# Kernel optimization log

Measured on AMD Instinct MI355X. Metric: run time of the kernel, lower is better.

Reference implementation:

```python
import jax, jax.numpy as jnp
import numpy as np
from math import factorial

MAXL = 5
TAUS = [8, 8, 8, 8, 8, 8]
OUT_TAUS = [8, 8, 8, 8, 8, 8]
BM_EPS = 1e-5
BATCH = 1024


def _cg_coeff(l1, l2, l, m1, m2, m):
    # Standard Clebsch-Gordan coefficient <l1 m1 l2 m2 | l m> (Racah formula).
    if m1 + m2 != m:
        return 0.0
    f = factorial
    pre = ((2 * l + 1) * f(l + l1 - l2) * f(l - l1 + l2) * f(l1 + l2 - l) / f(l1 + l2 + l + 1)) ** 0.5
    pre *= (f(l + m) * f(l - m) * f(l1 - m1) * f(l1 + m1) * f(l2 - m2) * f(l2 + m2)) ** 0.5
    s = 0.0
    for k in range(0, l1 + l2 - l + 1):
        ds = [k, l1 + l2 - l - k, l1 - m1 - k, l2 + m2 - k, l - l2 + m1 + k, l - l1 - m2 + k]
        if min(ds) < 0:
            continue
        d = 1.0
        for v in ds:
            d *= f(v)
        s += (-1.0) ** k / d
    return pre * s


def _cg_block(l1, l2, l):
    C = np.zeros((2 * l + 1, 2 * l1 + 1, 2 * l2 + 1), dtype=np.float32)
    for m in range(-l, l + 1):
        for m1 in range(-l1, l1 + 1):
            m2 = m - m1
            if -l2 <= m2 <= l2:
                C[m + l, m1 + l1, m2 + l2] = _cg_coeff(l1, l2, l, m1, m2, m)
    return C


# Triple enumeration order matches cal_middle_taus (l1 outer, l2, then l).
TRIPLES = []
for _l1 in range(MAXL + 1):
    for _l2 in range(_l1 + 1):
        for _l in range(_l1 - _l2, min(_l1 + _l2, MAXL) + 1):
            TRIPLES.append((_l1, _l2, _l))
CG_BLOCKS = [jnp.asarray(_cg_block(*t)) for t in TRIPLES]

MIDDLE_TAUS = np.zeros(MAXL + 1, dtype=np.int64)
for (_l1, _l2, _l) in TRIPLES:
    MIDDLE_TAUS[_l] += TAUS[_l1] * TAUS[_l2]
IN_LEN = int(sum(TAUS[l] * (2 * l + 1) for l in range(MAXL + 1)))    # 288
OUT_LEN = int(sum(OUT_TAUS[l] * (2 * l + 1) for l in range(MAXL + 1)))  # 288
WLEN = int(sum(OUT_TAUS[l] * int(MIDDLE_TAUS[l]) for l in range(MAXL + 1)))  # 35328
STD_LEN = int(MIDDLE_TAUS.sum())  # 4416


def _forward(activations, weights, moving_std):
    B = activations.shape[0]
    act = activations[..., 0] + 1j * activations[..., 1]  # [B, IN_LEN] complex64
    # split into per-degree blocks F[l]: [B, tau_l, 2l+1]
    F = []
    st = 0
    for l in range(MAXL + 1):
        n = TAUS[l] * (2 * l + 1)
        F.append(act[:, st:st + n].reshape(B, TAUS[l], 2 * l + 1))
        st += n
    # CG tensor product: one fragment per (l1,l2,l) triple, grouped by output degree l
    mids = [[] for _ in range(MAXL + 1)]
    for (l1, l2, l), C in zip(TRIPLES, CG_BLOCKS):
        frag = jnp.einsum('mac,bta,bsc->btsm', C.astype(act.dtype), F[l1], F[l2])
        mids[l].append(frag.reshape(B, TAUS[l1] * TAUS[l2], 2 * l + 1))
    # per-fragment batchnorm (divide by running std) + per-degree complex mixing
    outs = []
    so = 0
    wo = 0
    for l in range(MAXL + 1):
        mid = jnp.concatenate(mids[l], axis=1)  # [B, middle_taus[l], 2l+1]
        nt = int(MIDDLE_TAUS[l])
        std = moving_std[so:so + nt]
        so += nt
        mid = mid / (std + BM_EPS)[None, :, None]
        nw = OUT_TAUS[l] * nt
        wl = weights[wo:wo + nw]
        wo += nw
        Wc = (wl[:, 0] + 1j * wl[:, 1]).reshape(OUT_TAUS[l], nt)
        out = jnp.einsum('ot,btm->bom', Wc, mid)  # [B, out_taus[l], 2l+1]
        outs.append(out.reshape(B, OUT_TAUS[l] * (2 * l + 1)))
    oc = jnp.concatenate(outs, axis=1)  # [B, OUT_LEN] complex
    return jnp.stack([oc.real, oc.imag], axis=-1)  # [B, OUT_LEN, 2]


def setup_inputs() -> dict:
    key = jax.random.key(0)
    k1, k2, k3 = jax.random.split(key, 3)
    activations = jax.random.normal(k1, (BATCH, IN_LEN, 2), dtype=jnp.float32)
    weights = 0.05 * jax.random.uniform(k2, (WLEN, 2), dtype=jnp.float32)
    moving_std = 0.1 + 0.9 * jax.random.uniform(k3, (STD_LEN,), dtype=jnp.float32)
    return {"activations": activations, "weights": weights, "moving_std": moving_std}


def reference(activations, weights, moving_std):
    return _forward(activations, weights, moving_std)
```

## Files before the change

### kernel.cpp

```cpp
#include <hip/hip_runtime.h>
#include <hip/hip_bf16.h>
#include <utility>


constexpr int NTRIP = 69;
constexpr int NL    = 6;
constexpr int BATCH = 1024;
constexpr int ROW   = 288;
constexpr int MID_LDS = 4224;

struct Meta {
    int tl1[NTRIP], tl2[NTRIP], tll[NTRIP];
    int tf1[NTRIP], tf2[NTRIP];
    int ttloc[NTRIP];
    int trip_of_l[NL][16];
    int ntrips[NL];
    int mid_tau[NL], std_off[NL], w_off[NL], f_l[NL];
    int nch[NL];
    int ch_start[NL][2], ch_cnt[NL][2];
    int wave_of[NL][16];
};

constexpr Meta build_meta() {
    Meta m{};
    int fl[NL] = {};
    {
        int acc = 0;
        for (int l = 0; l < NL; l++) { fl[l] = acc; m.f_l[l] = acc; acc += 8 * (2 * l + 1); }
    }
    int idx = 0;
    for (int l1 = 0; l1 <= 5; l1++)
        for (int l2 = 0; l2 <= l1; l2++) {
            int lmax = (l1 + l2 < 5) ? (l1 + l2) : 5;
            for (int l = l1 - l2; l <= lmax; l++) {
                m.tl1[idx] = l1; m.tl2[idx] = l2; m.tll[idx] = l;
                m.tf1[idx] = fl[l1]; m.tf2[idx] = fl[l2];
                m.ttloc[idx] = 64 * m.ntrips[l];
                m.trip_of_l[l][m.ntrips[l]] = idx;
                m.ntrips[l]++;
                idx++;
            }
        }
    int so = 0, wo = 0;
    for (int l = 0; l < NL; l++) {
        m.mid_tau[l] = 64 * m.ntrips[l];
        m.std_off[l] = so; so += m.mid_tau[l];
        m.w_off[l]   = wo; wo += 8 * m.mid_tau[l];
    }
    for (int l = 0; l < NL; l++) {
        const int TW = 2 * l + 1;
        const int maxslot = MID_LDS / (64 * TW);
        const int ntl = m.ntrips[l];
        const int nch = (ntl + maxslot - 1) / maxslot;
        m.nch[l] = nch;
        int done = 0;
        for (int c = 0; c < nch; c++) {
            int cnt = (ntl - done + (nch - c) - 1) / (nch - c);
            m.ch_start[l][c] = done; m.ch_cnt[l][c] = cnt; done += cnt;
        }
        for (int c = 0; c < nch; c++) {
            const int s0 = m.ch_start[l][c], cnt = m.ch_cnt[l][c];
            int cost[16] = {}; bool asg[16] = {};
            for (int i = 0; i < cnt; i++) {
                int trip = m.trip_of_l[l][s0 + i];
                int l1 = m.tl1[trip], l2 = m.tl2[trip];
                int tc = 0;
                for (int mi = 0; mi < TW; mi++) {
                    int base = mi - l;
                    int lo = base + l1 - l2; if (lo < 0) lo = 0;
                    int hi = base + l1 + l2; if (hi > 2 * l1) hi = 2 * l1;
                    tc += hi - lo + 1;
                }
                cost[i] = tc * 6 + (2 * l1 + 1 + 2 * l2 + 1) * 2;
            }
            int load[4] = {};
            for (int k = 0; k < cnt; k++) {
                int best = -1, bc = -1;
                for (int i = 0; i < cnt; i++)
                    if (!asg[i] && cost[i] > bc) { bc = cost[i]; best = i; }
                asg[best] = true;
                int wsel = 0;
                for (int w2 = 1; w2 < 4; w2++) if (load[w2] < load[wsel]) wsel = w2;
                m.wave_of[l][s0 + best] = wsel;
                load[wsel] += bc;
            }
        }
    }
    return m;
}

constexpr Meta MT = build_meta();
constexpr int WLEN = 35328;
static_assert(MT.w_off[5] + 8 * MT.mid_tau[5] == WLEN, "wlen");
static_assert(MT.std_off[5] + MT.mid_tau[5] == 4416, "stdlen");

constexpr double cfact(int n) {
    double r = 1.0;
    for (int i = 2; i <= n; i++) r *= (double)i;
    return r;
}
constexpr double csqrt(double x) {
    double g = x > 1.0 ? x : 1.0;
    for (int i = 0; i < 100; i++) g = 0.5 * (g + x / g);
    return g;
}
constexpr float cg_coeff(int l1, int l2, int l, int m1, int m2, int m) {
    if (m1 + m2 != m) return 0.0f;
    double pre = csqrt((double)(2 * l + 1) * cfact(l + l1 - l2) * cfact(l - l1 + l2) *
                       cfact(l1 + l2 - l) / cfact(l1 + l2 + l + 1));
    pre *= csqrt(cfact(l + m) * cfact(l - m) * cfact(l1 - m1) * cfact(l1 + m1) *
                 cfact(l2 - m2) * cfact(l2 + m2));
    double s = 0.0;
    for (int k = 0; k <= l1 + l2 - l; k++) {
        int d0 = k, d1 = l1 + l2 - l - k, d2 = l1 - m1 - k;
        int d3 = l2 + m2 - k, d4 = l - l2 + m1 + k, d5 = l - l1 - m2 + k;
        if (d0 < 0 || d1 < 0 || d2 < 0 || d3 < 0 || d4 < 0 || d5 < 0) continue;
        double den = cfact(d0) * cfact(d1) * cfact(d2) * cfact(d3) * cfact(d4) * cfact(d5);
        s += ((k & 1) ? -1.0 : 1.0) / den;
    }
    return (float)(pre * s);
}

template <int... Is, class F>
__device__ __forceinline__ void static_for_impl(std::integer_sequence<int, Is...>, F&& f) {
    (f(std::integral_constant<int, Is>{}), ...);
}
template <int N, class F>
__device__ __forceinline__ void static_for(F&& f) {
    static_for_impl(std::make_integer_sequence<int, N>{}, (F&&)f);
}

template <int L>
__device__ __forceinline__ void process_l(int b, int tid,
                                          const float2* __restrict__ F,
                                          float2* __restrict__ mid,
                                          const float2* __restrict__ w,
                                          const float* __restrict__ stdv,
                                          float2* __restrict__ out) {
    constexpr int TW  = 2 * L + 1;
    constexpr int NCH = MT.nch[L];
    constexpr int NT  = MT.mid_tau[L];

    const int wid  = tid >> 6;
    const int lane = tid & 63;
    const int t = lane >> 3, s = lane & 7;

    float2 acc0[TW], acc1[TW];
#pragma unroll
    for (int i = 0; i < TW; i++) { acc0[i] = make_float2(0.f, 0.f); acc1[i] = make_float2(0.f, 0.f); }

    static_for<NCH>([&](auto CHc) {
        constexpr int CH  = decltype(CHc)::value;
        constexpr int S0  = MT.ch_start[L][CH];
        constexpr int CNT = MT.ch_cnt[L][CH];
        constexpr int CT  = CNT * 64;
        static_assert(CT * TW <= MID_LDS, "chunk fits");

        __syncthreads();

        static_for<CNT>([&](auto SIc) {
            constexpr int SI   = S0 + decltype(SIc)::value;
            constexpr int TRIP = MT.trip_of_l[L][SI];
            constexpr int L1   = MT.tl1[TRIP];
            constexpr int L2v  = MT.tl2[TRIP];
            constexpr int N1   = 2 * L1 + 1, N2 = 2 * L2v + 1;
            if (MT.wave_of[L][SI] == wid) {
                const float inv = 1.0f /
                    (stdv[MT.std_off[L] + MT.ttloc[TRIP] + lane] + 1e-5f);
                const float2* F1 = F + MT.tf1[TRIP] + t * N1;
                const float2* F2 = F + MT.tf2[TRIP] + s * N2;
                float2 f1[N1], f2[N2];
#pragma unroll
                for (int i = 0; i < N1; i++) f1[i] = F1[i];
#pragma unroll
                for (int i = 0; i < N2; i++) f2[i] = F2[i];
                const int Tloc = (MT.ttloc[TRIP] - S0 * 64) + lane;
                static_for<TW>([&](auto MIc) {
                    constexpr int MI   = decltype(MIc)::value;
                    constexpr int BASE = MI - L;
                    constexpr int LO_  = BASE + L1 - L2v;
                    constexpr int LO   = LO_ < 0 ? 0 : LO_;
                    constexpr int HI_  = BASE + L1 + L2v;
                    constexpr int HI   = HI_ > 2 * L1 ? 2 * L1 : HI_;
                    float re = 0.f, im = 0.f;
                    static_for<HI - LO + 1>([&](auto Kc) {
                        constexpr int AI = LO + decltype(Kc)::value;
                        constexpr int CI = BASE + L1 + L2v - AI;
                        constexpr float cv = cg_coeff(L1, L2v, L, AI - L1, CI - L2v, BASE);
                        if constexpr (cv != 0.0f) {
                            const float2 a = f1[AI], c2 = f2[CI];
                            re = fmaf(cv, fmaf(-a.y, c2.y, a.x * c2.x), re);
                            im = fmaf(cv, fmaf(a.y, c2.x, a.x * c2.y), im);
                        }
                    });
                    mid[MI * CT + Tloc] = make_float2(re * inv, im * inv);
                });
            }
        });
        __syncthreads();

        {
            constexpr int NIT = (CT + 127) / 128;
            const float2* W0 = w + MT.w_off[L] + wid * NT + S0 * 64;
            const float2* W1 = w + MT.w_off[L] + (wid + 4) * NT + S0 * 64;
            float4 wA[NIT], wB[NIT];
            static_for<NIT>([&](auto Ic) {
                constexpr int I = decltype(Ic)::value;
                const int T = lane * 2 + I * 128;
                if constexpr ((I + 1) * 128 <= CT) {
                    wA[I] = *reinterpret_cast<const float4*>(W0 + T);
                    wB[I] = *reinterpret_cast<const float4*>(W1 + T);
                } else {
                    if (T < CT) {
                        wA[I] = *reinterpret_cast<const float4*>(W0 + T);
                        wB[I] = *reinterpret_cast<const float4*>(W1 + T);
                    }
                }
            });
            static_for<NIT>([&](auto Ic) {
                constexpr int I = decltype(Ic)::value;
                const int T = lane * 2 + I * 128;
                const float4 w0 = wA[I], w1 = wB[I];
                auto body = [&]() {
#pragma unroll
                    for (int mi = 0; mi < TW; mi++) {
                        const float4 mv = *reinterpret_cast<const float4*>(mid + mi * CT + T);
                        acc0[mi].x = fmaf(w0.x, mv.x, fmaf(-w0.y, mv.y,
                                      fmaf(w0.z, mv.z, fmaf(-w0.w, mv.w, acc0[mi].x))));
                        acc0[mi].y = fmaf(w0.x, mv.y, fmaf(w0.y, mv.x,
                                      fmaf(w0.z, mv.w, fmaf(w0.w, mv.z, acc0[mi].y))));
                        acc1[mi].x = fmaf(w1.x, mv.x, fmaf(-w1.y, mv.y,
                                      fmaf(w1.z, mv.z, fmaf(-w1.w, mv.w, acc1[mi].x))));
                        acc1[mi].y = fmaf(w1.x, mv.y, fmaf(w1.y, mv.x,
                                      fmaf(w1.z, mv.w, fmaf(w1.w, mv.z, acc1[mi].y))));
                    }
                };
                if constexpr ((I + 1) * 128 <= CT) body();
                else { if (T < CT) body(); }
            });
        }
    });

    const bool lo = (lane < 32);
    float2 red[TW];
#pragma unroll
    for (int mi = 0; mi < TW; mi++) {
        float gx = lo ? acc1[mi].x : acc0[mi].x;
        float gy = lo ? acc1[mi].y : acc0[mi].y;
        float rx = (lo ? acc0[mi].x : acc1[mi].x) + __shfl_xor(gx, 32, 64);
        float ry = (lo ? acc0[mi].y : acc1[mi].y) + __shfl_xor(gy, 32, 64);
#pragma unroll
        for (int off = 16; off >= 1; off >>= 1) {
            rx += __shfl_xor(rx, off, 64);
            ry += __shfl_xor(ry, off, 64);
        }
        red[mi] = make_float2(rx, ry);
    }
    if (lane == 0 || lane == 32) {
        const int o = wid + (lo ? 0 : 4);
        float2* orow = out + (size_t)b * ROW + MT.f_l[L] + o * TW;
#pragma unroll
        for (int mi = 0; mi < TW; mi++) orow[mi] = red[mi];
    }
}

__global__ __launch_bounds__(256, 4) void fup_main(const float2* __restrict__ act,
                                                   const float2* __restrict__ w,
                                                   const float* __restrict__ stdv,
                                                   float2* __restrict__ out) {
    __shared__ float2 F[ROW];
    __shared__ __align__(16) float2 mid[MID_LDS];
    const int b = blockIdx.x;
    const int tid = threadIdx.x;
    const float2* arow = act + (size_t)b * ROW;
    for (int i = tid; i < ROW; i += 256) F[i] = arow[i];
    process_l<0>(b, tid, F, mid, w, stdv, out);
    process_l<1>(b, tid, F, mid, w, stdv, out);
    process_l<2>(b, tid, F, mid, w, stdv, out);
    process_l<3>(b, tid, F, mid, w, stdv, out);
    process_l<4>(b, tid, F, mid, w, stdv, out);
    process_l<5>(b, tid, F, mid, w, stdv, out);
}

extern "C" void kernel_launch(void* const* d_in, const int* in_sizes, int n_in,
                              void* d_out, int out_size, void* d_ws, size_t ws_size,
                              hipStream_t stream) {
    const float2* act  = (const float2*)d_in[0];
    const float2* wts  = (const float2*)d_in[1];
    const float*  stdv = (const float*)d_in[2];
    float2* out = (float2*)d_out;
    (void)d_ws; (void)ws_size;

    hipLaunchKernelGGL(fup_main, dim3(BATCH), dim3(256), 0, stream,
                       act, wts, stdv, out);
}
```

Measured before the change: 138.2 us.

## Split each batch row across two blocks by degree group, halve mid LDS

Each batch row is now processed by two blocks: one handles output degrees 0,1,2,5 and the other handles 3,4, with the groups balanced by chunk count. The grid doubles, the mid LDS buffer is halved, and launch bounds rise to 8 blocks per CU to increase occupancy and parallelism. The weight-load loop becomes a runtime loop instead of a fully prefetched static_for, which reduces register pressure but drops the early weight-load batching. Each block redundantly loads the activation row, and the chunking metadata is widened to support smaller chunks.

After: 343.1 us. +148.3%, slower.

```diff
diff --git a/kernel.cpp b/kernel.cpp
--- a/kernel.cpp
+++ b/kernel.cpp
@@ -7,7 +7,7 @@
 constexpr int NL    = 6;
 constexpr int BATCH = 1024;
 constexpr int ROW   = 288;
-constexpr int MID_LDS = 4224;
+constexpr int MID_LDS = 2112;
 
 struct Meta {
     int tl1[NTRIP], tl2[NTRIP], tll[NTRIP];
@@ -17,7 +17,7 @@
     int ntrips[NL];
     int mid_tau[NL], std_off[NL], w_off[NL], f_l[NL];
     int nch[NL];
-    int ch_start[NL][2], ch_cnt[NL][2];
+    int ch_start[NL][8], ch_cnt[NL][8];
     int wave_of[NL][16];
 };
 
@@ -93,6 +93,8 @@
 constexpr int WLEN = 35328;
 static_assert(MT.w_off[5] + 8 * MT.mid_tau[5] == WLEN, "wlen");
 static_assert(MT.std_off[5] + MT.mid_tau[5] == 4416, "stdlen");
+static_assert(MT.nch[0] + MT.nch[1] + MT.nch[2] + MT.nch[5] == 9, "grpA");
+static_assert(MT.nch[3] + MT.nch[4] == 9, "grpB");
 
 constexpr double cfact(int n) {
     double r = 1.0;
@@ -200,44 +202,24 @@
         __syncthreads();
 
         {
-            constexpr int NIT = (CT + 127) / 128;
             const float2* W0 = w + MT.w_off[L] + wid * NT + S0 * 64;
             const float2* W1 = w + MT.w_off[L] + (wid + 4) * NT + S0 * 64;
-            float4 wA[NIT], wB[NIT];
-            static_for<NIT>([&](auto Ic) {
-                constexpr int I = decltype(Ic)::value;
-                const int T = lane * 2 + I * 128;
-                if constexpr ((I + 1) * 128 <= CT) {
-                    wA[I] = *reinterpret_cast<const float4*>(W0 + T);
-                    wB[I] = *reinterpret_cast<const float4*>(W1 + T);
-                } else {
-                    if (T < CT) {
-                        wA[I] = *reinterpret_cast<const float4*>(W0 + T);
-                        wB[I] = *reinterpret_cast<const float4*>(W1 + T);
-                    }
+            for (int T = lane * 2; T < CT; T += 128) {
+                const float4 w0 = *reinterpret_cast<const float4*>(W0 + T);
+                const float4 w1 = *reinterpret_cast<const float4*>(W1 + T);
+#pragma unroll
+                for (int mi = 0; mi < TW; mi++) {
+                    const float4 mv = *reinterpret_cast<const float4*>(mid + mi * CT + T);
+                    acc0[mi].x = fmaf(w0.x, mv.x, fmaf(-w0.y, mv.y,
+                                  fmaf(w0.z, mv.z, fmaf(-w0.w, mv.w, acc0[mi].x))));
+                    acc0[mi].y = fmaf(w0.x, mv.y, fmaf(w0.y, mv.x,
+                                  fmaf(w0.z, mv.w, fmaf(w0.w, mv.z, acc0[mi].y))));
+                    acc1[mi].x = fmaf(w1.x, mv.x, fmaf(-w1.y, mv.y,
+                                  fmaf(w1.z, mv.z, fmaf(-w1.w, mv.w, acc1[mi].x))));
+                    acc1[mi].y = fmaf(w1.x, mv.y, fmaf(w1.y, mv.x,
+                                  fmaf(w1.z, mv.w, fmaf(w1.w, mv.z, acc1[mi].y))));
                 }
-            });
-            static_for<NIT>([&](auto Ic) {
-                constexpr int I = decltype(Ic)::value;
-                const int T = lane * 2 + I * 128;
-                const float4 w0 = wA[I], w1 = wB[I];
-                auto body = [&]() {
-#pragma unroll
-                    for (int mi = 0; mi < TW; mi++) {
-                        const float4 mv = *reinterpret_cast<const float4*>(mid + mi * CT + T);
-                        acc0[mi].x = fmaf(w0.x, mv.x, fmaf(-w0.y, mv.y,
-                                      fmaf(w0.z, mv.z, fmaf(-w0.w, mv.w, acc0[mi].x))));
-                        acc0[mi].y = fmaf(w0.x, mv.y, fmaf(w0.y, mv.x,
-                                      fmaf(w0.z, mv.w, fmaf(w0.w, mv.z, acc0[mi].y))));
-                        acc1[mi].x = fmaf(w1.x, mv.x, fmaf(-w1.y, mv.y,
-                                      fmaf(w1.z, mv.z, fmaf(-w1.w, mv.w, acc1[mi].x))));
-                        acc1[mi].y = fmaf(w1.x, mv.y, fmaf(w1.y, mv.x,
-                                      fmaf(w1.z, mv.w, fmaf(w1.w, mv.z, acc1[mi].y))));
-                    }
-                };
-                if constexpr ((I + 1) * 128 <= CT) body();
-                else { if (T < CT) body(); }
-            });
+            }
         }
     });
 
@@ -264,22 +246,27 @@
     }
 }
 
-__global__ __launch_bounds__(256, 4) void fup_main(const float2* __restrict__ act,
+__global__ __launch_bounds__(256, 8) void fup_main(const float2* __restrict__ act,
                                                    const float2* __restrict__ w,
                                                    const float* __restrict__ stdv,
                                                    float2* __restrict__ out) {
     __shared__ float2 F[ROW];
     __shared__ __align__(16) float2 mid[MID_LDS];
-    const int b = blockIdx.x;
+    const int bid = blockIdx.x;
+    const int grp = bid & 1;
+    const int b   = bid >> 1;
     const int tid = threadIdx.x;
     const float2* arow = act + (size_t)b * ROW;
     for (int i = tid; i < ROW; i += 256) F[i] = arow[i];
-    process_l<0>(b, tid, F, mid, w, stdv, out);
-    process_l<1>(b, tid, F, mid, w, stdv, out);
-    process_l<2>(b, tid, F, mid, w, stdv, out);
-    process_l<3>(b, tid, F, mid, w, stdv, out);
-    process_l<4>(b, tid, F, mid, w, stdv, out);
-    process_l<5>(b, tid, F, mid, w, stdv, out);
+    if (grp == 0) {
+        process_l<0>(b, tid, F, mid, w, stdv, out);
+        process_l<1>(b, tid, F, mid, w, stdv, out);
+        process_l<2>(b, tid, F, mid, w, stdv, out);
+        process_l<5>(b, tid, F, mid, w, stdv, out);
+    } else {
+        process_l<3>(b, tid, F, mid, w, stdv, out);
+        process_l<4>(b, tid, F, mid, w, stdv, out);
+    }
 }
 
 extern "C" void kernel_launch(void* const* d_in, const int* in_sizes, int n_in,
@@ -291,6 +278,6 @@
     float2* out = (float2*)d_out;
     (void)d_ws; (void)ws_size;
 
-    hipLaunchKernelGGL(fup_main, dim3(BATCH), dim3(256), 0, stream,
+    hipLaunchKernelGGL(fup_main, dim3(2 * BATCH), dim3(256), 0, stream,
                        act, wts, stdv, out);
 }
```
